# Optimization experiments

Measured on AMD Instinct MI355X. Metric: run time of the kernel, lower is better.

Reference implementation:

```python
import jax, jax.numpy as jnp
import numpy as np

# ---- dims (mirror reconstructed HybridSignToTextModel) ----
INPUT_SIZE = 256
CONV_CH = 512
ENC_HID = 512          # per-direction encoder GRU hidden
ENC_OUT = 2 * ENC_HID  # bidirectional concat = 1024
DEC_LAYERS = 2
DEC_HID = 512
EMB = 512
VOCAB = 8000
ATTN = 512
MAX_DEC = 50
SOS, EOS, PAD = 1, 2, 0


def _gru_cell(x, h, Wih, Whh, bih, bhh):
    # torch GRUCell math. x:(B,I) h:(B,H) Wih:(3H,I) Whh:(3H,H)
    gi = x @ Wih.T + bih
    gh = h @ Whh.T + bhh
    H = h.shape[-1]
    ir, iz, inn = gi[:, :H], gi[:, H:2*H], gi[:, 2*H:]
    hr, hz, hn = gh[:, :H], gh[:, H:2*H], gh[:, 2*H:]
    r = jax.nn.sigmoid(ir + hr)
    z = jax.nn.sigmoid(iz + hz)
    n = jnp.tanh(inn + r * hn)
    return (1.0 - z) * n + z * h


def _gru_layer(xs, h0, Wih, Whh, bih, bhh, reverse=False):
    # xs: (T,B,I) -> outputs (T,B,H), final h (B,H)
    def step(h, x):
        h = _gru_cell(x, h, Wih, Whh, bih, bhh)
        return h, h
    hT, ys = jax.lax.scan(step, h0, xs, reverse=reverse)
    return ys, hT


def _conv1d(x, w, b, stride):
    # x:(B,C,T) w:(O,C,K) 'same'-ish padding K//2
    k = w.shape[-1]
    y = jax.lax.conv_general_dilated(x, w, (stride,), [(k // 2, k // 2)],
                                     dimension_numbers=("NCH", "OIH", "NCH"))
    return y + b[None, :, None]


def setup_inputs() -> dict:
    key = jax.random.key(0)
    ks = iter(jax.random.split(key, 40))
    def rn(shape, s=0.05):
        return (jax.random.normal(next(ks), shape, dtype=jnp.float32) * s)
    p = {}
    p["features"] = jax.random.normal(next(ks), (32, 512, INPUT_SIZE), dtype=jnp.float32)
    # conv encoder: 2 conv1d layers, stride 2 each, ReLU
    p["conv_w1"] = rn((CONV_CH, INPUT_SIZE, 5)); p["conv_b1"] = rn((CONV_CH,))
    p["conv_w2"] = rn((CONV_CH, CONV_CH, 5)); p["conv_b2"] = rn((CONV_CH,))
    # bidirectional encoder GRU (1 layer)
    for d in ("f", "b"):
        p[f"enc_Wih_{d}"] = rn((3 * ENC_HID, CONV_CH))
        p[f"enc_Whh_{d}"] = rn((3 * ENC_HID, ENC_HID))
        p[f"enc_bih_{d}"] = rn((3 * ENC_HID,))
        p[f"enc_bhh_{d}"] = rn((3 * ENC_HID,))
    # hidden bridge: 2*ENC_HID -> DEC_LAYERS*DEC_HID
    p["bridge_W"] = rn((DEC_LAYERS * DEC_HID, 2 * ENC_HID)); p["bridge_b"] = rn((DEC_LAYERS * DEC_HID,))
    # decoder embedding
    p["emb"] = rn((VOCAB, EMB), 0.1)
    # Bahdanau attention
    p["attn_We"] = rn((ATTN, ENC_OUT)); p["attn_Wd"] = rn((ATTN, DEC_HID)); p["attn_v"] = rn((ATTN,))
    # decoder GRU: 2 layers; layer0 in = EMB+ENC_OUT, layer1 in = DEC_HID
    ins = [EMB + ENC_OUT, DEC_HID]
    for l in range(DEC_LAYERS):
        p[f"dec_Wih{l}"] = rn((3 * DEC_HID, ins[l]))
        p[f"dec_Whh{l}"] = rn((3 * DEC_HID, DEC_HID))
        p[f"dec_bih{l}"] = rn((3 * DEC_HID,))
        p[f"dec_bhh{l}"] = rn((3 * DEC_HID,))
    # output proj: DEC_HID + ENC_OUT -> VOCAB
    p["proj_W"] = rn((VOCAB, DEC_HID + ENC_OUT)); p["proj_b"] = rn((VOCAB,))
    return p


def reference(features, conv_w1, conv_b1, conv_w2, conv_b2,
              enc_Wih_f, enc_Whh_f, enc_bih_f, enc_bhh_f,
              enc_Wih_b, enc_Whh_b, enc_bih_b, enc_bhh_b,
              bridge_W, bridge_b, emb, attn_We, attn_Wd, attn_v,
              dec_Wih0, dec_Whh0, dec_bih0, dec_bhh0,
              dec_Wih1, dec_Whh1, dec_bih1, dec_bhh1,
              proj_W, proj_b):
    B = features.shape[0]
    # ---- conv encoder ----
    x = features.transpose(0, 2, 1)                 # (B,C,T)
    x = jax.nn.relu(_conv1d(x, conv_w1, conv_b1, 2))
    x = jax.nn.relu(_conv1d(x, conv_w2, conv_b2, 2))
    x = x.transpose(2, 0, 1)                        # (T',B,C)
    # ---- bidirectional GRU encoder ----
    h0 = jnp.zeros((B, ENC_HID), features.dtype)
    yf, hf = _gru_layer(x, h0, enc_Wih_f, enc_Whh_f, enc_bih_f, enc_bhh_f)
    yb, hb = _gru_layer(x, h0, enc_Wih_b, enc_Whh_b, enc_bih_b, enc_bhh_b, reverse=True)
    enc_out = jnp.concatenate([yf, yb], -1).transpose(1, 0, 2)   # (B,T',2H)
    combined = jnp.concatenate([hf, hb], -1)                      # (B,2H)
    dec_h = (combined @ bridge_W.T + bridge_b).reshape(B, DEC_LAYERS, DEC_HID).transpose(1, 0, 2)
    # precompute attention keys
    enc_proj = jnp.einsum("bte,ae->bta", enc_out, attn_We)       # (B,T',A)

    def attention(h_top):
        score = jnp.einsum("bta,a->bt", jnp.tanh(enc_proj + (h_top @ attn_Wd.T)[:, None, :]), attn_v)
        w = jax.nn.softmax(score, axis=-1)
        return jnp.einsum("bt,bte->be", w, enc_out)               # (B,2H)

    def decode_step(carry, _):
        tok, h = carry                                            # h: (L,B,H)
        e = emb[tok]                                              # (B,EMB)
        ctx = attention(h[-1])
        g0 = _gru_cell(jnp.concatenate([e, ctx], -1), h[0], dec_Wih0, dec_Whh0, dec_bih0, dec_bhh0)
        g1 = _gru_cell(g0, h[1], dec_Wih1, dec_Whh1, dec_bih1, dec_bhh1)
        logits = jnp.concatenate([g1, ctx], -1) @ proj_W.T + proj_b
        nxt = jnp.argmax(logits, -1)
        return (nxt, jnp.stack([g0, g1])), nxt

    init_tok = jnp.full((B,), SOS, dtype=jnp.int32)
    _, toks = jax.lax.scan(decode_step, (init_tok, dec_h), None, length=MAX_DEC - 1)
    decoded = jnp.concatenate([init_tok[:, None], toks.T], axis=1)  # (B,MAX_DEC)
    return decoded
```

## Files before the change

kernel.cpp:

```cpp
#include <hip/hip_runtime.h>
#include <math.h>

#define DINLINE __device__ __forceinline__

DINLINE float sigmoidf_(float x) { return 1.f / (1.f + expf(-x)); }

__device__ __align__(256) float g_ws[36200000];

__device__ unsigned g_cnt;
__device__ unsigned g_epoch;
__device__ __align__(128) unsigned g_sub[16 * 32];

#define GRID_BAR()                                                          \
  do {                                                                      \
    __syncthreads();                                                        \
    if (threadIdx.x == 0) {                                                 \
      __threadfence();                                                      \
      bar_target += 1u;                                                     \
      unsigned prev_ = atomicAdd(&g_cnt, 1u);                               \
      if (prev_ == 255u) {                                                  \
        atomicExch(&g_cnt, 0u);                                             \
        __threadfence();                                                    \
        atomicExch(&g_epoch, bar_target);                                   \
      }                                                                     \
      if ((blockIdx.x & 15) == 0) {                                         \
        while (atomicAdd(&g_epoch, 0u) < bar_target)                        \
          __builtin_amdgcn_s_sleep(16);                                     \
        atomicExch(&g_sub[(blockIdx.x >> 4) * 32], bar_target);             \
      } else {                                                              \
        while (atomicAdd(&g_sub[(blockIdx.x >> 4) * 32], 0u) < bar_target)  \
          __builtin_amdgcn_s_sleep(16);                                     \
      }                                                                     \
      __threadfence();                                                      \
    }                                                                       \
    __syncthreads();                                                        \
  } while (0)

__global__ void reset_bar_kernel() {
  int i = threadIdx.x;
  if (i == 0) { g_cnt = 0u; g_epoch = 0u; }
  if (i < 16) g_sub[i * 32] = 0u;
}

__global__ void im2col1_kernel(const float* __restrict__ feat, float* __restrict__ P) {
  size_t i = (size_t)blockIdx.x * 256 + threadIdx.x;
  int col = (int)(i % 1280);
  int row = (int)(i / 1280);
  int c = col / 5, k = col - c * 5;
  int l = row & 255, b = row >> 8;
  int pos = 2 * l + k - 2;
  P[i] = (pos >= 0 && pos < 512) ? feat[((size_t)b * 512 + pos) * 256 + c] : 0.f;
}

__global__ void im2col2_kernel(const float* __restrict__ y1, float* __restrict__ P) {
  size_t i = (size_t)blockIdx.x * 256 + threadIdx.x;
  int col = (int)(i % 2560);
  int row = (int)(i / 2560);
  int c = col / 5, k = col - c * 5;
  int l = row & 127, b = row >> 7;
  int pos = 2 * l + k - 2;
  P[i] = (pos >= 0 && pos < 256) ? y1[((size_t)b * 256 + pos) * 512 + c] : 0.f;
}

__global__ __launch_bounds__(256) void sgemm128(
    const float* __restrict__ A, const float* __restrict__ B,
    const float* __restrict__ bias, float* __restrict__ C,
    int M, int N, int K, int relu) {
  __shared__ float As[8][132];
  __shared__ float Bs[8][132];
  int bm = blockIdx.y * 128, bn = blockIdx.x * 128;
  int tid = threadIdx.x;
  int tx = tid & 15, ty = tid >> 4;
  float acc[8][8];
#pragma unroll
  for (int i = 0; i < 8; ++i)
#pragma unroll
    for (int j = 0; j < 8; ++j) acc[i][j] = 0.f;
  int lr = tid >> 1;
  int lc = (tid & 1) * 4;
  const float* Arow = A + (size_t)(bm + lr) * K + lc;
  const float* Brow = B + (size_t)(bn + lr) * K + lc;
  for (int k0 = 0; k0 < K; k0 += 8) {
    float4 av = *(const float4*)(Arow + k0);
    float4 bv = *(const float4*)(Brow + k0);
    As[lc + 0][lr] = av.x; As[lc + 1][lr] = av.y; As[lc + 2][lr] = av.z; As[lc + 3][lr] = av.w;
    Bs[lc + 0][lr] = bv.x; Bs[lc + 1][lr] = bv.y; Bs[lc + 2][lr] = bv.z; Bs[lc + 3][lr] = bv.w;
    __syncthreads();
#pragma unroll
    for (int kk = 0; kk < 8; ++kk) {
      float4 a0 = *(const float4*)&As[kk][ty * 8];
      float4 a1 = *(const float4*)&As[kk][ty * 8 + 4];
      float4 b0 = *(const float4*)&Bs[kk][tx * 8];
      float4 b1 = *(const float4*)&Bs[kk][tx * 8 + 4];
      float aa[8] = {a0.x, a0.y, a0.z, a0.w, a1.x, a1.y, a1.z, a1.w};
      float bb[8] = {b0.x, b0.y, b0.z, b0.w, b1.x, b1.y, b1.z, b1.w};
#pragma unroll
      for (int i = 0; i < 8; ++i)
#pragma unroll
        for (int j = 0; j < 8; ++j) acc[i][j] += aa[i] * bb[j];
    }
    __syncthreads();
  }
#pragma unroll
  for (int i = 0; i < 8; ++i) {
    int m = bm + ty * 8 + i;
#pragma unroll
    for (int j = 0; j < 8; ++j) {
      int n = bn + tx * 8 + j;
      float v = acc[i][j] + (bias ? bias[n] : 0.f);
      if (relu) v = fmaxf(v, 0.f);
      C[(size_t)m * N + n] = v;
    }
  }
}

__global__ __launch_bounds__(1024) void enc_persist2(
    const float* __restrict__ gi_f, const float* __restrict__ gi_b,
    const float* __restrict__ Whh_f, const float* __restrict__ bhh_f,
    const float* __restrict__ Whh_b, const float* __restrict__ bhh_b,
    float* __restrict__ h_fin, float* __restrict__ enc_out) {
  __shared__ float hcur[512];
  __shared__ float gh[1536];
  int swz = blockIdx.x & 7;
  int dir = swz >> 2;
  int b = ((blockIdx.x >> 3) << 2) | (swz & 3);
  int tid = threadIdx.x;
  int sl = tid & 7, nl = tid >> 3;
  const float* gi  = dir ? gi_b  : gi_f;
  const float* Whh = dir ? Whh_b : Whh_f;
  const float* bhh = dir ? bhh_b : bhh_f;
  float bhr = 0.f, bhz = 0.f, bhn = 0.f;
  if (tid < 512) {
    hcur[tid] = 0.f;
    bhr = bhh[tid]; bhz = bhh[512 + tid]; bhn = bhh[1024 + tid];
  }
  __syncthreads();
  for (int s = 0; s < 128; ++s) {
    int t = dir ? (127 - s) : s;
#pragma unroll 2
    for (int pass = 0; pass < 12; ++pass) {
      int m = pass * 128 + nl;
      const float4* wp = (const float4*)(Whh + (size_t)m * 512);
      float a = 0.f;
#pragma unroll
      for (int q = 0; q < 16; ++q) {
        float4 wv = wp[q * 8 + sl];
        float4 hv = *(const float4*)&hcur[(q * 8 + sl) * 4];
        a += wv.x * hv.x + wv.y * hv.y + wv.z * hv.z + wv.w * hv.w;
      }
      a += __shfl_xor(a, 1);
      a += __shfl_xor(a, 2);
      a += __shfl_xor(a, 4);
      if (sl == 0) gh[m] = a;
    }
    __syncthreads();
    if (tid < 512) {
      int j = tid;
      const float* g = gi + ((size_t)b * 128 + t) * 1536;
      float r = sigmoidf_(g[j] + gh[j] + bhr);
      float z = sigmoidf_(g[512 + j] + gh[512 + j] + bhz);
      float n = tanhf(g[1024 + j] + r * (gh[1024 + j] + bhn));
      float hnew = (1.f - z) * n + z * hcur[j];
      hcur[j] = hnew;
      enc_out[((size_t)b * 128 + t) * 1024 + dir * 512 + j] = hnew;
    }
    __syncthreads();
  }
  if (tid < 512) h_fin[dir * 16384 + b * 512 + tid] = hcur[tid];
}

__global__ __launch_bounds__(256) void gemvB(
    const float* __restrict__ A1, const int* __restrict__ tokidx, int len1,
    const float* __restrict__ A2, int len2,
    const float* __restrict__ W, const float* __restrict__ bias,
    float* __restrict__ out0, float* __restrict__ out1, int split, int N, int K) {
  int tid = threadIdx.x;
  int s = tid & 7, nl = tid >> 3;
  int n = blockIdx.x * 32 + nl;
  __shared__ float4 xs4[32 * 32];
  float acc[32];
#pragma unroll
  for (int b = 0; b < 32; ++b) acc[b] = 0.f;
  const float4* W4 = (const float4*)(W + (size_t)n * K);
  int K4 = K >> 2;
  int len1_4 = len1 >> 2;
  for (int k0 = 0; k0 < K4; k0 += 32) {
    __syncthreads();
    for (int idx = tid; idx < 1024; idx += 256) {
      int b = idx >> 5, kf = idx & 31;
      int gk = k0 + kf;
      float4 v;
      if (gk < len1_4) {
        const float* src = tokidx ? (A1 + (size_t)tokidx[b] * len1) : (A1 + (size_t)b * len1);
        v = ((const float4*)src)[gk];
      } else {
        v = ((const float4*)(A2 + (size_t)b * len2))[gk - len1_4];
      }
      xs4[idx] = v;
    }
    __syncthreads();
    const float4* wp = W4 + k0;
#pragma unroll
    for (int j = 0; j < 4; ++j) {
      float4 wv = wp[j * 8 + s];
      const float4* xp = xs4 + j * 8 + s;
#pragma unroll
      for (int b = 0; b < 32; ++b) {
        float4 xv = xp[b * 32];
        acc[b] += wv.x * xv.x + wv.y * xv.y + wv.z * xv.z + wv.w * xv.w;
      }
    }
  }
#pragma unroll
  for (int b = 0; b < 32; ++b) {
    float v = acc[b];
    v += __shfl_xor(v, 1);
    v += __shfl_xor(v, 2);
    v += __shfl_xor(v, 4);
    acc[b] = v;
  }
  if (s == 0) {
    float bv = bias ? bias[n] : 0.f;
#pragma unroll
    for (int b = 0; b < 32; ++b) {
      float val = acc[b] + bv;
      if (n < split) out0[(size_t)b * split + n] = val;
      else out1[(size_t)b * (N - split) + (n - split)] = val;
    }
  }
}

__global__ __launch_bounds__(256) void dec_persist(
    const float* __restrict__ emb, const float* __restrict__ attn_Wd,
    const float* __restrict__ attn_v,
    const float* __restrict__ enc_pj, const float* __restrict__ enc_out,
    const float* __restrict__ dec_Wih0, const float* __restrict__ dec_bih0,
    const float* __restrict__ dec_Whh0, const float* __restrict__ dec_bhh0,
    const float* __restrict__ dec_Wih1, const float* __restrict__ dec_bih1,
    const float* __restrict__ dec_Whh1, const float* __restrict__ dec_bhh1,
    const float* __restrict__ proj_W, const float* __restrict__ proj_b,
    float* __restrict__ h0d, float* __restrict__ h1d,
    float* __restrict__ ctxb, float* __restrict__ dbuf,
    unsigned long long* __restrict__ keys, int* __restrict__ tok,
    int* __restrict__ decoded) {
  __shared__ float4 SB[1024];
  __shared__ unsigned long long ksh[32 * 33];
  __shared__ float d_s[512];
  __shared__ float red_s[256];
  __shared__ float sc_s[128];
  unsigned bar_target = 0u;
  int blk = blockIdx.x, tid = threadIdx.x;
  int s8 = tid & 7, nl = tid >> 3;
  int bb31 = tid & 31, jj = tid >> 5;

  for (int s = 0; s < 49; ++s) {
    int cur = s & 1, nxt = (s + 1) & 1;
    const float* h1cur = h1d + cur * 16384;

    if (blk < 16) {
      int n = blk * 32 + nl;
      float acc[32];
#pragma unroll
      for (int b = 0; b < 32; ++b) acc[b] = 0.f;
      const float4* W4 = (const float4*)(attn_Wd + (size_t)n * 512);
      for (int k0 = 0; k0 < 128; k0 += 32) {
        __syncthreads();
        for (int idx = tid; idx < 1024; idx += 256) {
          int b = idx >> 5, kf = idx & 31;
          SB[idx] = ((const float4*)(h1cur + (size_t)b * 512))[k0 + kf];
        }
        __syncthreads();
        const float4* wp = W4 + k0;
#pragma unroll
        for (int j = 0; j < 4; ++j) {
          float4 wv = wp[j * 8 + s8];
          const float4* xp = SB + j * 8 + s8;
#pragma unroll
          for (int b = 0; b < 32; ++b) {
            float4 xv = xp[b * 32];
            acc[b] += wv.x * xv.x + wv.y * xv.y + wv.z * xv.z + wv.w * xv.w;
          }
        }
      }
#pragma unroll
      for (int b = 0; b < 32; ++b) {
        float v = acc[b];
        v += __shfl_xor(v, 1);
        v += __shfl_xor(v, 2);
        v += __shfl_xor(v, 4);
        if (s8 == 0) dbuf[(size_t)b * 512 + n] = v;
      }
    } else if (blk == 16 && s > 0 && tid < 32) {
      unsigned long long k = keys[tid];
      int n = (int)(0xFFFFFFFFu - (unsigned)(k & 0xFFFFFFFFull));
      tok[tid] = n;
      decoded[tid * 50 + s] = n;
    }
    GRID_BAR();

    if (blk < 32) {
      int b = blk;
      d_s[tid] = dbuf[b * 512 + tid];
      d_s[tid + 256] = dbuf[b * 512 + tid + 256];
      __syncthreads();
      {
        int t = tid >> 1, part = tid & 1;
        const float* ep = enc_pj + ((size_t)b * 128 + t) * 512 + part * 256;
        const float* dd = d_s + part * 256;
        const float* vv = attn_v + part * 256;
        float sv = 0.f;
        for (int a = 0; a < 256; ++a) sv += tanhf(ep[a] + dd[a]) * vv[a];
        red_s[tid] = sv;
      }
      __syncthreads();
      if (tid < 128) sc_s[tid] = red_s[tid * 2] + red_s[tid * 2 + 1];
      __syncthreads();
      if (tid == 0) {
        float m = -1e30f;
        for (int t = 0; t < 128; ++t) m = fmaxf(m, sc_s[t]);
        float sum = 0.f;
        for (int t = 0; t < 128; ++t) { float e = expf(sc_s[t] - m); sc_s[t] = e; sum += e; }
        float inv = 1.f / sum;
        for (int t = 0; t < 128; ++t) sc_s[t] *= inv;
      }
      __syncthreads();
      for (int e = tid; e < 1024; e += 256) {
        const float* eo = enc_out + (size_t)b * 131072 + e;
        float sv = 0.f;
        for (int t = 0; t < 128; ++t) sv += sc_s[t] * eo[(size_t)t * 1024];
        ctxb[b * 1024 + e] = sv;
      }
    } else if (blk == 32 && tid < 32) {
      keys[tid] = 0ULL;
    }
    GRID_BAR();

    for (int layer = 0; layer < 2; ++layer) {
      if (blk < 64) {
        const float* A1   = layer ? (h0d + nxt * 16384) : emb;
        const int* tki    = layer ? (const int*)0 : tok;
        int len1          = 512;
        const float* A2   = layer ? (const float*)0 : ctxb;
        int len2          = layer ? 0 : 1024;
        const float* Wih  = layer ? dec_Wih1 : dec_Wih0;
        const float* bih  = layer ? dec_bih1 : dec_bih0;
        const float* Whh  = layer ? dec_Whh1 : dec_Whh0;
        const float* bhh  = layer ? dec_bhh1 : dec_bhh0;
        const float* h_in = layer ? (h1d + cur * 16384) : (h0d + cur * 16384);
        float* h_out      = layer ? (h1d + nxt * 16384) : (h0d + nxt * 16384);
        int b = bb31, j = (blk << 3) + jj;
        int Kin = len1 + len2;
        int K4 = Kin >> 2, len1_4 = len1 >> 2;
        int sw5 = b & 31;
        const float4* wir = (const float4*)(Wih + (size_t)j * Kin);
        const float4* wiz = (const float4*)(Wih + (size_t)(512 + j) * Kin);
        const float4* win = (const float4*)(Wih + (size_t)(1024 + j) * Kin);
        float gr = 0.f, gz = 0.f, gn = 0.f;
        for (int k0 = 0; k0 < K4; k0 += 32) {
          __syncthreads();
          for (int idx = tid; idx < 1024; idx += 256) {
            int bs = idx >> 5, kf = idx & 31;
            int gk = k0 + kf;
            float4 v;
            if (gk < len1_4) {
              const float* src = tki ? (A1 + (size_t)tki[bs] * len1) : (A1 + (size_t)bs * len1);
              v = ((const float4*)src)[gk];
            } else {
              v = ((const float4*)(A2 + (size_t)bs * len2))[gk - len1_4];
            }
            SB[(bs << 5) + (kf ^ (bs & 31))] = v;
          }
          __syncthreads();
          const float4* xrow = SB + (b << 5);
          const float4* wr_ = wir + k0;
          const float4* wz_ = wiz + k0;
          const float4* wn_ = win + k0;
#pragma unroll 4
          for (int kf = 0; kf < 32; ++kf) {
            float4 xv = xrow[kf ^ sw5];
            float4 r4 = wr_[kf];
            float4 z4 = wz_[kf];
            float4 n4 = wn_[kf];
            gr += xv.x * r4.x + xv.y * r4.y + xv.z * r4.z + xv.w * r4.w;
            gz += xv.x * z4.x + xv.y * z4.y + xv.z * z4.z + xv.w * z4.w;
            gn += xv.x * n4.x + xv.y * n4.y + xv.z * n4.z + xv.w * n4.w;
          }
        }
        const float4* whr = (const float4*)(Whh + (size_t)j * 512);
        const float4* whz = (const float4*)(Whh + (size_t)(512 + j) * 512);
        const float4* whn = (const float4*)(Whh + (size_t)(1024 + j) * 512);
        float sr = 0.f, sz = 0.f, sn = 0.f;
        for (int k0 = 0; k0 < 128; k0 += 32) {
          __syncthreads();
          for (int idx = tid; idx < 1024; idx += 256) {
            int bs = idx >> 5, kf = idx & 31;
            float4 v = ((const float4*)(h_in + (size_t)bs * 512))[k0 + kf];
            SB[(bs << 5) + (kf ^ (bs & 31))] = v;
          }
          __syncthreads();
          const float4* xrow = SB + (b << 5);
          const float4* wr_ = whr + k0;
          const float4* wz_ = whz + k0;
          const float4* wn_ = whn + k0;
#pragma unroll 4
          for (int kf = 0; kf < 32; ++kf) {
            float4 xv = xrow[kf ^ sw5];
            float4 r4 = wr_[kf];
            float4 z4 = wz_[kf];
            float4 n4 = wn_[kf];
            sr += xv.x * r4.x + xv.y * r4.y + xv.z * r4.z + xv.w * r4.w;
            sz += xv.x * z4.x + xv.y * z4.y + xv.z * z4.z + xv.w * z4.w;
            sn += xv.x * n4.x + xv.y * n4.y + xv.z * n4.z + xv.w * n4.w;
          }
        }
        float r = sigmoidf_(gr + bih[j] + sr + bhh[j]);
        float z = sigmoidf_(gz + bih[512 + j] + sz + bhh[512 + j]);
        float n = tanhf(gn + bih[1024 + j] + r * (sn + bhh[1024 + j]));
        float hj = h_in[b * 512 + j];
        h_out[b * 512 + j] = (1.f - z) * n + z * hj;
      }
      GRID_BAR();
    }

    if (blk < 250) {
      const float* h1n = h1d + nxt * 16384;
      int n = blk * 32 + nl;
      float acc[32];
#pragma unroll
      for (int b = 0; b < 32; ++b) acc[b] = 0.f;
      const float4* W4 = (const float4*)(proj_W + (size_t)n * 1536);
      for (int k0 = 0; k0 < 384; k0 += 32) {
        __syncthreads();
        for (int idx = tid; idx < 1024; idx += 256) {
          int b = idx >> 5, kf = idx & 31;
          int gk = k0 + kf;
          float4 v;
          if (gk < 128) v = ((const float4*)(h1n + (size_t)b * 512))[gk];
          else v = ((const float4*)(ctxb + (size_t)b * 1024))[gk - 128];
          SB[idx] = v;
        }
        __syncthreads();
        const float4* wp = W4 + k0;
#pragma unroll
        for (int j = 0; j < 4; ++j) {
          float4 wv = wp[j * 8 + s8];
          const float4* xp = SB + j * 8 + s8;
#pragma unroll
          for (int b = 0; b < 32; ++b) {
            float4 xv = xp[b * 32];
            acc[b] += wv.x * xv.x + wv.y * xv.y + wv.z * xv.z + wv.w * xv.w;
          }
        }
      }
#pragma unroll
      for (int b = 0; b < 32; ++b) {
        float v = acc[b];
        v += __shfl_xor(v, 1);
        v += __shfl_xor(v, 2);
        v += __shfl_xor(v, 4);
        acc[b] = v;
      }
      if (s8 == 0) {
        float bv = proj_b[n];
#pragma unroll
        for (int b = 0; b < 32; ++b) {
          float val = acc[b] + bv;
          unsigned u = __float_as_uint(val);
          u = (u & 0x80000000u) ? ~u : (u | 0x80000000u);
          ksh[nl * 33 + b] =
              ((unsigned long long)u << 32) | (unsigned long long)(0xFFFFFFFFu - (unsigned)n);
        }
      }
      __syncthreads();
      if (tid < 32) {
        unsigned long long best = 0ULL;
#pragma unroll 8
        for (int q = 0; q < 32; ++q) {
          unsigned long long v = ksh[q * 33 + tid];
          if (v > best) best = v;
        }
        atomicMax(&keys[tid], best);
      }
      __syncthreads();
    }
    GRID_BAR();
  }
  if (blk == 0 && tid < 32) {
    unsigned long long k = keys[tid];
    decoded[tid * 50 + 49] = (int)(0xFFFFFFFFu - (unsigned)(k & 0xFFFFFFFFull));
  }
}

__global__ void init_kernel(int* __restrict__ tok, int* __restrict__ decoded) {
  int b = threadIdx.x;
  if (b >= 32) return;
  tok[b] = 1;
  decoded[b * 50] = 1;
}

extern "C" void kernel_launch(void* const* d_in, const int* in_sizes, int n_in,
                              void* d_out, int out_size, void* d_ws, size_t ws_size,
                              hipStream_t stream) {
  const float* features  = (const float*)d_in[0];
  const float* conv_w1   = (const float*)d_in[1];
  const float* conv_b1   = (const float*)d_in[2];
  const float* conv_w2   = (const float*)d_in[3];
  const float* conv_b2   = (const float*)d_in[4];
  const float* enc_Wih_f = (const float*)d_in[5];
  const float* enc_Whh_f = (const float*)d_in[6];
  const float* enc_bih_f = (const float*)d_in[7];
  const float* enc_bhh_f = (const float*)d_in[8];
  const float* enc_Wih_b = (const float*)d_in[9];
  const float* enc_Whh_b = (const float*)d_in[10];
  const float* enc_bih_b = (const float*)d_in[11];
  const float* enc_bhh_b = (const float*)d_in[12];
  const float* bridge_W  = (const float*)d_in[13];
  const float* bridge_b  = (const float*)d_in[14];
  const float* emb       = (const float*)d_in[15];
  const float* attn_We   = (const float*)d_in[16];
  const float* attn_Wd   = (const float*)d_in[17];
  const float* attn_v    = (const float*)d_in[18];
  const float* dec_Wih0  = (const float*)d_in[19];
  const float* dec_Whh0  = (const float*)d_in[20];
  const float* dec_bih0  = (const float*)d_in[21];
  const float* dec_bhh0  = (const float*)d_in[22];
  const float* dec_Wih1  = (const float*)d_in[23];
  const float* dec_Whh1  = (const float*)d_in[24];
  const float* dec_bih1  = (const float*)d_in[25];
  const float* dec_bhh1  = (const float*)d_in[26];
  const float* proj_W    = (const float*)d_in[27];
  const float* proj_b    = (const float*)d_in[28];
  int* decoded = (int*)d_out;

  float* ws = nullptr;
  hipGetSymbolAddress((void**)&ws, HIP_SYMBOL(g_ws));
  float* P       = ws;
  float* y1      = ws + 10485760;
  float* x2      = ws + 14680064;
  float* gi_f    = ws + 16777216;
  float* gi_b    = ws + 23068672;
  float* enc_out = ws + 29360128;
  float* enc_pj  = ws + 33554432;
  float* h_enc   = ws + 35651584;
  float* h0d     = ws + 35717120;
  float* h1d     = ws + 35749888;
  float* ctxb    = ws + 35782656;
  unsigned long long* keys = (unsigned long long*)(ws + 35815424);
  int*   tok     = (int*)(ws + 35815488);
  float* dbuf    = ws + 35815520;

  im2col1_kernel<<<40960, 256, 0, stream>>>(features, P);
  sgemm128<<<dim3(4, 64), 256, 0, stream>>>(P, conv_w1, conv_b1, y1, 8192, 512, 1280, 1);
  im2col2_kernel<<<40960, 256, 0, stream>>>(y1, P);
  sgemm128<<<dim3(4, 32), 256, 0, stream>>>(P, conv_w2, conv_b2, x2, 4096, 512, 2560, 1);

  sgemm128<<<dim3(12, 32), 256, 0, stream>>>(x2, enc_Wih_f, enc_bih_f, gi_f, 4096, 1536, 512, 0);
  sgemm128<<<dim3(12, 32), 256, 0, stream>>>(x2, enc_Wih_b, enc_bih_b, gi_b, 4096, 1536, 512, 0);

  enc_persist2<<<64, 1024, 0, stream>>>(gi_f, gi_b,
      enc_Whh_f, enc_bhh_f, enc_Whh_b, enc_bhh_b, h_enc, enc_out);

  gemvB<<<32, 256, 0, stream>>>(h_enc, nullptr, 512, h_enc + 16384, 512,
      bridge_W, bridge_b, h0d, h1d, 512, 1024, 1024);

  sgemm128<<<dim3(4, 32), 256, 0, stream>>>(enc_out, attn_We, nullptr, enc_pj, 4096, 512, 1024, 0);

  init_kernel<<<1, 64, 0, stream>>>(tok, decoded);
  reset_bar_kernel<<<1, 64, 0, stream>>>();

  dec_persist<<<256, 256, 0, stream>>>(emb, attn_Wd, attn_v, enc_pj, enc_out,
      dec_Wih0, dec_bih0, dec_Whh0, dec_bhh0,
      dec_Wih1, dec_bih1, dec_Whh1, dec_bhh1,
      proj_W, proj_b, h0d, h1d, ctxb, dbuf, keys, tok, decoded);
}
```

Baseline: 20.79 ms.

## Fuse attention query GEMV into attention blocks, removing a grid barrier per step

Each of the 32 attention blocks now computes its own batch row of h_top @ attn_Wd.T in shared memory, instead of a separate 16-block GEMV phase followed by a grid-wide barrier. Token extraction moves into the attention phase, so each decode step has one fewer barrier. The grid barrier becomes a two-level arrival tree with shorter sleeps, and the projection GEMM stages larger K chunks (96 float4) to cut its sync count. The cost is that attn_Wd is read redundantly by 32 blocks (about 1MB each per step) and shared memory use grows.

```diff
diff --git a/kernel.cpp b/kernel.cpp
--- a/kernel.cpp
+++ b/kernel.cpp
@@ -9,6 +9,7 @@
 
 __device__ unsigned g_cnt;
 __device__ unsigned g_epoch;
+__device__ __align__(128) unsigned g_arr[16 * 32];
 __device__ __align__(128) unsigned g_sub[16 * 32];
 
 #define GRID_BAR()                                                          \
@@ -17,19 +18,24 @@
     if (threadIdx.x == 0) {                                                 \
       __threadfence();                                                      \
       bar_target += 1u;                                                     \
-      unsigned prev_ = atomicAdd(&g_cnt, 1u);                               \
-      if (prev_ == 255u) {                                                  \
-        atomicExch(&g_cnt, 0u);                                             \
-        __threadfence();                                                    \
-        atomicExch(&g_epoch, bar_target);                                   \
+      int grp_ = blockIdx.x >> 4;                                           \
+      unsigned p_ = atomicAdd(&g_arr[grp_ * 32], 1u);                       \
+      if (p_ == 15u) {                                                      \
+        atomicExch(&g_arr[grp_ * 32], 0u);                                  \
+        unsigned q_ = atomicAdd(&g_cnt, 1u);                                \
+        if (q_ == 15u) {                                                    \
+          atomicExch(&g_cnt, 0u);                                           \
+          __threadfence();                                                  \
+          atomicExch(&g_epoch, bar_target);                                 \
+        }                                                                   \
       }                                                                     \
       if ((blockIdx.x & 15) == 0) {                                         \
         while (atomicAdd(&g_epoch, 0u) < bar_target)                        \
-          __builtin_amdgcn_s_sleep(16);                                     \
-        atomicExch(&g_sub[(blockIdx.x >> 4) * 32], bar_target);             \
+          __builtin_amdgcn_s_sleep(8);                                      \
+        atomicExch(&g_sub[grp_ * 32], bar_target);                          \
       } else {                                                              \
-        while (atomicAdd(&g_sub[(blockIdx.x >> 4) * 32], 0u) < bar_target)  \
-          __builtin_amdgcn_s_sleep(16);                                     \
+        while (atomicAdd(&g_sub[grp_ * 32], 0u) < bar_target)               \
+          __builtin_amdgcn_s_sleep(8);                                      \
       }                                                                     \
       __threadfence();                                                      \
     }                                                                       \
@@ -39,7 +45,7 @@
 __global__ void reset_bar_kernel() {
   int i = threadIdx.x;
   if (i == 0) { g_cnt = 0u; g_epoch = 0u; }
-  if (i < 16) g_sub[i * 32] = 0u;
+  if (i < 16) { g_arr[i * 32] = 0u; g_sub[i * 32] = 0u; }
 }
 
 __global__ void im2col1_kernel(const float* __restrict__ feat, float* __restrict__ P) {
@@ -240,12 +246,13 @@
     const float* __restrict__ dec_Whh1, const float* __restrict__ dec_bhh1,
     const float* __restrict__ proj_W, const float* __restrict__ proj_b,
     float* __restrict__ h0d, float* __restrict__ h1d,
-    float* __restrict__ ctxb, float* __restrict__ dbuf,
+    float* __restrict__ ctxb,
     unsigned long long* __restrict__ keys, int* __restrict__ tok,
     int* __restrict__ decoded) {
-  __shared__ float4 SB[1024];
+  __shared__ float4 SB[3072];
   __shared__ unsigned long long ksh[32 * 33];
   __shared__ float d_s[512];
+  __shared__ float hb_s[512];
   __shared__ float red_s[256];
   __shared__ float sc_s[128];
   unsigned bar_target = 0u;
@@ -257,51 +264,26 @@
     int cur = s & 1, nxt = (s + 1) & 1;
     const float* h1cur = h1d + cur * 16384;
 
-    if (blk < 16) {
-      int n = blk * 32 + nl;
-      float acc[32];
-#pragma unroll
-      for (int b = 0; b < 32; ++b) acc[b] = 0.f;
-      const float4* W4 = (const float4*)(attn_Wd + (size_t)n * 512);
-      for (int k0 = 0; k0 < 128; k0 += 32) {
-        __syncthreads();
-        for (int idx = tid; idx < 1024; idx += 256) {
-          int b = idx >> 5, kf = idx & 31;
-          SB[idx] = ((const float4*)(h1cur + (size_t)b * 512))[k0 + kf];
-        }
-        __syncthreads();
-        const float4* wp = W4 + k0;
-#pragma unroll
-        for (int j = 0; j < 4; ++j) {
-          float4 wv = wp[j * 8 + s8];
-          const float4* xp = SB + j * 8 + s8;
-#pragma unroll
-          for (int b = 0; b < 32; ++b) {
-            float4 xv = xp[b * 32];
-            acc[b] += wv.x * xv.x + wv.y * xv.y + wv.z * xv.z + wv.w * xv.w;
-          }
-        }
-      }
-#pragma unroll
-      for (int b = 0; b < 32; ++b) {
-        float v = acc[b];
-        v += __shfl_xor(v, 1);
-        v += __shfl_xor(v, 2);
-        v += __shfl_xor(v, 4);
-        if (s8 == 0) dbuf[(size_t)b * 512 + n] = v;
-      }
-    } else if (blk == 16 && s > 0 && tid < 32) {
-      unsigned long long k = keys[tid];
-      int n = (int)(0xFFFFFFFFu - (unsigned)(k & 0xFFFFFFFFull));
-      tok[tid] = n;
-      decoded[tid * 50 + s] = n;
-    }
-    GRID_BAR();
-
     if (blk < 32) {
       int b = blk;
-      d_s[tid] = dbuf[b * 512 + tid];
-      d_s[tid + 256] = dbuf[b * 512 + tid + 256];
+      hb_s[tid] = h1cur[b * 512 + tid];
+      hb_s[tid + 256] = h1cur[b * 512 + 256 + tid];
+      __syncthreads();
+      for (int pass = 0; pass < 16; ++pass) {
+        int a = pass * 32 + nl;
+        const float4* wp = (const float4*)(attn_Wd + (size_t)a * 512);
+        float sum = 0.f;
+#pragma unroll
+        for (int q = 0; q < 16; ++q) {
+          float4 wv = wp[q * 8 + s8];
+          float4 hv = *(const float4*)&hb_s[(q * 8 + s8) * 4];
+          sum += wv.x * hv.x + wv.y * hv.y + wv.z * hv.z + wv.w * hv.w;
+        }
+        sum += __shfl_xor(sum, 1);
+        sum += __shfl_xor(sum, 2);
+        sum += __shfl_xor(sum, 4);
+        if (s8 == 0) d_s[a] = sum;
+      }
       __syncthreads();
       {
         int t = tid >> 1, part = tid & 1;
@@ -331,6 +313,12 @@
         ctxb[b * 1024 + e] = sv;
       }
     } else if (blk == 32 && tid < 32) {
+      if (s > 0) {
+        unsigned long long k = keys[tid];
+        int n = (int)(0xFFFFFFFFu - (unsigned)(k & 0xFFFFFFFFull));
+        tok[tid] = n;
+        decoded[tid * 50 + s] = n;
+      }
       keys[tid] = 0ULL;
     }
     GRID_BAR();
@@ -429,25 +417,28 @@
 #pragma unroll
       for (int b = 0; b < 32; ++b) acc[b] = 0.f;
       const float4* W4 = (const float4*)(proj_W + (size_t)n * 1536);
-      for (int k0 = 0; k0 < 384; k0 += 32) {
+      for (int c = 0; c < 4; ++c) {
         __syncthreads();
-        for (int idx = tid; idx < 1024; idx += 256) {
-          int b = idx >> 5, kf = idx & 31;
-          int gk = k0 + kf;
+#pragma unroll
+        for (int r = 0; r < 12; ++r) {
+          int e = r * 256 + tid;
+          int bb = e / 96;
+          int kk = e - bb * 96;
+          int gk = c * 96 + kk;
           float4 v;
-          if (gk < 128) v = ((const float4*)(h1n + (size_t)b * 512))[gk];
-          else v = ((const float4*)(ctxb + (size_t)b * 1024))[gk - 128];
-          SB[idx] = v;
+          if (gk < 128) v = ((const float4*)(h1n + (size_t)bb * 512))[gk];
+          else v = ((const float4*)(ctxb + (size_t)bb * 1024))[gk - 128];
+          SB[bb * 96 + kk] = v;
         }
         __syncthreads();
-        const float4* wp = W4 + k0;
-#pragma unroll
-        for (int j = 0; j < 4; ++j) {
+        const float4* wp = W4 + c * 96;
+#pragma unroll
+        for (int j = 0; j < 12; ++j) {
           float4 wv = wp[j * 8 + s8];
           const float4* xp = SB + j * 8 + s8;
 #pragma unroll
           for (int b = 0; b < 32; ++b) {
-            float4 xv = xp[b * 32];
+            float4 xv = xp[b * 96];
             acc[b] += wv.x * xv.x + wv.y * xv.y + wv.z * xv.z + wv.w * xv.w;
           }
         }
@@ -547,7 +538,6 @@
   float* ctxb    = ws + 35782656;
   unsigned long long* keys = (unsigned long long*)(ws + 35815424);
   int*   tok     = (int*)(ws + 35815488);
-  float* dbuf    = ws + 35815520;
 
   im2col1_kernel<<<40960, 256, 0, stream>>>(features, P);
   sgemm128<<<dim3(4, 64), 256, 0, stream>>>(P, conv_w1, conv_b1, y1, 8192, 512, 1280, 1);
@@ -571,5 +561,5 @@
   dec_persist<<<256, 256, 0, stream>>>(emb, attn_Wd, attn_v, enc_pj, enc_out,
       dec_Wih0, dec_bih0, dec_Whh0, dec_bhh0,
       dec_Wih1, dec_bih1, dec_Whh1, dec_bhh1,
-      proj_W, proj_b, h0d, h1d, ctxb, dbuf, keys, tok, decoded);
-}
+      proj_W, proj_b, h0d, h1d, ctxb, keys, tok, decoded);
+}
```

Result: slower. 25.86 ms (+24.4%).
